# Performance work log

Measured on AMD Instinct MI355X. Metric: run time of the kernel, lower is better.

## Reference

```python
import jax, jax.numpy as jnp
import numpy as np

B, T, E, D = 32, 8192, 256, 32  # batch, seq, embed_dim, output_dim
H, M = D, 2 * D                 # SSM hidden_dim, mlp_dim


def _ssm_block(x, Win, bin_, log_a, Wout, bout, W1, b1, W2, b2):
    """Diagonal linear SSM scan + residual MLP. x: (B,T,D) -> (B,T,D)."""
    u = x @ Win + bin_                      # (B,T,H)
    a = jax.nn.sigmoid(log_a)               # (H,) per-channel decay in (0,1)
    aa = jnp.broadcast_to(a, u.shape)

    def comb(c1, c2):
        a1, h1 = c1
        a2, h2 = c2
        return a1 * a2, a2 * h1 + h2

    _, h = jax.lax.associative_scan(comb, (aa, u), axis=1)  # h_t = a*h_{t-1} + u_t
    y = h @ Wout + bout                      # (B,T,D)
    return y + jax.nn.gelu(y @ W1 + b1) @ W2 + b2


def setup_inputs() -> dict:
    key = jax.random.key(0)
    ks = jax.random.split(key, 20)
    s_in, s_d, s_m = 1.0 / np.sqrt(E), 1.0 / np.sqrt(D), 1.0 / np.sqrt(M)
    inp = {
        "e_seq": jax.random.normal(ks[0], (B, T, E), dtype=jnp.float32),
        "Wpi": jax.random.normal(ks[1], (E, D), dtype=jnp.float32) * s_in,
        "bpi": jnp.zeros((D,), jnp.float32),
        "Wpo": jax.random.normal(ks[2], (2 * D, D), dtype=jnp.float32) * s_d,
        "bpo": jnp.zeros((D,), jnp.float32),
    }
    for i, pfx in enumerate(["f", "b"]):
        o = 3 + 8 * i
        inp[pfx + "_Win"] = jax.random.normal(ks[o], (D, H), dtype=jnp.float32) * s_d
        inp[pfx + "_bin"] = jnp.zeros((H,), jnp.float32)
        inp[pfx + "_loga"] = jax.random.normal(ks[o + 1], (H,), dtype=jnp.float32)
        inp[pfx + "_Wout"] = jax.random.normal(ks[o + 2], (H, D), dtype=jnp.float32) * s_d
        inp[pfx + "_bout"] = jnp.zeros((D,), jnp.float32)
        inp[pfx + "_W1"] = jax.random.normal(ks[o + 3], (D, M), dtype=jnp.float32) * s_d
        inp[pfx + "_b1"] = jnp.zeros((M,), jnp.float32)
        inp[pfx + "_W2"] = jax.random.normal(ks[o + 4], (M, D), dtype=jnp.float32) * s_m
        inp[pfx + "_b2"] = jnp.zeros((D,), jnp.float32)
    return inp


def reference(e_seq, Wpi, bpi, Wpo, bpo,
              f_Win, f_bin, f_loga, f_Wout, f_bout, f_W1, f_b1, f_W2, f_b2,
              b_Win, b_bin, b_loga, b_Wout, b_bout, b_W1, b_b1, b_W2, b_b2):
    x = e_seq @ Wpi + bpi                                    # (B,T,D)
    fwd = _ssm_block(x, f_Win, f_bin, f_loga, f_Wout, f_bout, f_W1, f_b1, f_W2, f_b2)
    bwd = _ssm_block(x[:, ::-1], b_Win, b_bin, b_loga, b_Wout, b_bout,
                     b_W1, b_b1, b_W2, b_b2)[:, ::-1]
    combined = jnp.concatenate([fwd, bwd], axis=-1)           # (B,T,2D)
    return combined @ Wpo + bpo                               # (B,T,D)
```

## Files before the change

kernel.cpp:

```cpp
#include <hip/hip_runtime.h>


typedef unsigned short u16;
typedef unsigned int   u32;
typedef __bf16 bf16x8 __attribute__((ext_vector_type(8)));
typedef float  f32x4  __attribute__((ext_vector_type(4)));

constexpr int BB = 32, TT = 8192, EE = 256, DD = 32, NCH = 64;
constexpr int BT = BB * TT;
constexpr int LCH = 256;
constexpr int NCHUNK = TT / LCH;
constexpr int SUBLEN = 64;

__device__ __forceinline__ u16 f2bf(float x) {
    union { float f; u32 u; } v; v.f = x;
    u32 r = (v.u + 0x7FFFu + ((v.u >> 16) & 1u)) >> 16;
    return (u16)r;
}
__device__ __forceinline__ float bf2f(u16 x) {
    union { u32 u; float f; } v; v.u = ((u32)x) << 16;
    return v.f;
}
__device__ __forceinline__ float gelu_tanh(float x) {
    float inner = 0.7978845608028654f * fmaf(0.044715f * x, x * x, x);
    float ez = __expf(2.f * inner);
    float t = 1.f - 2.f / (ez + 1.f);
    return 0.5f * x * (1.f + t);
}

__global__ void k0_prep(const float* __restrict__ Wpi, const float* __restrict__ bpi,
                        const float* __restrict__ fWin, const float* __restrict__ fbin,
                        const float* __restrict__ floga,
                        const float* __restrict__ bWin, const float* __restrict__ bbin,
                        const float* __restrict__ bloga,
                        const float* __restrict__ fW1, const float* __restrict__ bW1,
                        const float* __restrict__ fW2, const float* __restrict__ bW2,
                        const float* __restrict__ fb2, const float* __restrict__ bb2,
                        const float* __restrict__ Wpo, const float* __restrict__ bpo,
                        u16* __restrict__ WuT, float* __restrict__ bu,
                        float* __restrict__ a_arr, float* __restrict__ l2a,
                        float* __restrict__ fW1T, float* __restrict__ bW1T,
                        float* __restrict__ W2poF, float* __restrict__ W2poB,
                        float* __restrict__ bc)
{
    const int blk = blockIdx.x, tid = threadIdx.x;
    if (blk < 64) {
        const float* Win = (blk < 32) ? fWin : bWin;
        const int nn = blk & 31;
        float s = 0.f;
        #pragma unroll
        for (int d = 0; d < 32; ++d) s = fmaf(Wpi[tid * 32 + d], Win[d * 32 + nn], s);
        WuT[blk * 256 + tid] = f2bf(s);
        if (tid == 0) {
            const float* bin = (blk < 32) ? fbin : bbin;
            float sb = bin[nn];
            for (int d = 0; d < 32; ++d) sb = fmaf(bpi[d], Win[d * 32 + nn], sb);
            bu[blk] = sb;
        }
    } else if (blk == 64) {
        if (tid < 64) {
            const float* lg = (tid < 32) ? floga : bloga;
            float a = 1.f / (1.f + __expf(-lg[tid & 31]));
            a_arr[tid] = a;
            l2a[tid] = log2f(a);
        } else if (tid < 96) {
            int i = tid - 64;
            float s = bpo[i];
            for (int d = 0; d < 32; ++d) s = fmaf(fb2[d], Wpo[d * 32 + i], s);
            for (int d = 0; d < 32; ++d) s = fmaf(bb2[d], Wpo[(32 + d) * 32 + i], s);
            bc[i] = s;
        }
    } else if (blk == 65 || blk == 66) {
        const float* W1 = (blk == 65) ? fW1 : bW1;
        float* W1T = (blk == 65) ? fW1T : bW1T;
        for (int x = tid; x < 2048; x += 256) {
            int j = x >> 5, i = x & 31;
            W1T[j * 32 + i] = W1[i * 64 + j];
        }
    } else {
        const float* W2 = (blk == 67) ? fW2 : bW2;
        const float* Wp = (blk == 67) ? Wpo : (Wpo + 32 * 32);
        float* Dst = (blk == 67) ? W2poF : W2poB;
        for (int x = tid; x < 2048; x += 256) {
            int j = x >> 5, i = x & 31;
            float s = 0.f;
            for (int d = 0; d < 32; ++d) s = fmaf(W2[j * 32 + d], Wp[d * 32 + i], s);
            Dst[j * 32 + i] = s;
        }
    }
}

__global__ __launch_bounds__(256) void k1_proj(const float* __restrict__ e,
                                               const u16* __restrict__ WuT,
                                               const float* __restrict__ bu,
                                               u16* __restrict__ u)
{
    __shared__ __align__(16) u16 As[64][264];
    const int tid = threadIdx.x;
    const size_t m0 = (size_t)blockIdx.x * 64;

    const float4* eg = reinterpret_cast<const float4*>(e + m0 * 256);
    #pragma unroll
    for (int it = 0; it < 16; ++it) {
        int i = tid + it * 256;
        int r = i >> 6, kk = (i & 63) << 2;
        float4 v = eg[i];
        uint2 pk;
        pk.x = (u32)f2bf(v.x) | ((u32)f2bf(v.y) << 16);
        pk.y = (u32)f2bf(v.z) | ((u32)f2bf(v.w) << 16);
        *reinterpret_cast<uint2*>(&As[r][kk]) = pk;
    }
    __syncthreads();

    const int lane = tid & 63, wave = tid >> 6;
    const int row16 = lane & 15, quad = lane >> 4;
    f32x4 acc[4] = {{0.f,0.f,0.f,0.f},{0.f,0.f,0.f,0.f},{0.f,0.f,0.f,0.f},{0.f,0.f,0.f,0.f}};

    #pragma unroll 2
    for (int ks = 0; ks < 8; ++ks) {
        bf16x8 av = *reinterpret_cast<const bf16x8*>(&As[wave * 16 + row16][ks * 32 + quad * 8]);
        #pragma unroll
        for (int ct = 0; ct < 4; ++ct) {
            bf16x8 bv = *reinterpret_cast<const bf16x8*>(WuT + (ct * 16 + row16) * 256 + ks * 32 + quad * 8);
            acc[ct] = __builtin_amdgcn_mfma_f32_16x16x32_bf16(av, bv, acc[ct], 0, 0, 0);
        }
    }
    #pragma unroll
    for (int ct = 0; ct < 4; ++ct) {
        int col = ct * 16 + row16;
        float bias = bu[col];
        #pragma unroll
        for (int r = 0; r < 4; ++r) {
            int row = wave * 16 + quad * 4 + r;
            u[(m0 + row) * 64 + col] = f2bf(acc[ct][r] + bias);
        }
    }
}

__global__ __launch_bounds__(256) void k2_scan(u16* __restrict__ u,
                                               const float* __restrict__ a_arr,
                                               const float* __restrict__ l2a,
                                               float* __restrict__ Ebuf)
{
    __shared__ __align__(16) u16 tile[LCH * 64];
    __shared__ float eSub[64][4];
    const int tid = threadIdx.x;
    const int b = blockIdx.x >> 5, c = blockIdx.x & 31;
    const size_t base = (((size_t)b << 13) + ((size_t)c << 8)) * 64;

    const uint4* g = reinterpret_cast<const uint4*>(u + base);
    uint4* s4 = reinterpret_cast<uint4*>(tile);
    #pragma unroll
    for (int i = 0; i < 8; ++i) s4[tid + 256 * i] = g[tid + 256 * i];
    __syncthreads();

    const int ch = tid & 63, s = tid >> 6;
    const float a = a_arr[ch];
    const bool fwd = (ch < 32);

    float h = 0.f;
    if (fwd) {
        for (int i = 0; i < SUBLEN; ++i) {
            int t = s * SUBLEN + i;
            h = fmaf(a, h, bf2f(tile[t * 64 + ch]));
            tile[t * 64 + ch] = f2bf(h);
        }
    } else {
        for (int i = SUBLEN - 1; i >= 0; --i) {
            int t = s * SUBLEN + i;
            h = fmaf(a, h, bf2f(tile[t * 64 + ch]));
            tile[t * 64 + ch] = f2bf(h);
        }
    }
    eSub[ch][s] = h;
    __syncthreads();

    const float A = exp2f(64.f * l2a[ch]);
    float cin = 0.f;
    if (fwd) { for (int j = 0; j < s; ++j)      cin = fmaf(A, cin, eSub[ch][j]); }
    else     { for (int j = 3; j > s; --j)      cin = fmaf(A, cin, eSub[ch][j]); }

    if (fwd && s == 3)  Ebuf[(size_t)blockIdx.x * 64 + ch] = fmaf(A, cin, eSub[ch][3]);
    if (!fwd && s == 0) Ebuf[(size_t)blockIdx.x * 64 + ch] = fmaf(A, cin, eSub[ch][0]);

    float p = cin;
    if (fwd) {
        for (int i = 0; i < SUBLEN; ++i) {
            int t = s * SUBLEN + i; p *= a;
            tile[t * 64 + ch] = f2bf(bf2f(tile[t * 64 + ch]) + p);
        }
    } else {
        for (int i = SUBLEN - 1; i >= 0; --i) {
            int t = s * SUBLEN + i; p *= a;
            tile[t * 64 + ch] = f2bf(bf2f(tile[t * 64 + ch]) + p);
        }
    }
    __syncthreads();
    uint4* gw = reinterpret_cast<uint4*>(u + base);
    #pragma unroll
    for (int i = 0; i < 8; ++i) gw[tid + 256 * i] = s4[tid + 256 * i];
}

__global__ void k3_carry(const float* __restrict__ Ebuf, float* __restrict__ Cin,
                         const float* __restrict__ l2a)
{
    int tid = blockIdx.x * 256 + threadIdx.x;
    if (tid >= BB * NCH) return;
    int b = tid >> 6, ch = tid & 63;
    float aL = exp2f((float)LCH * l2a[ch]);
    float S = 0.f;
    if (ch < 32) {
        for (int c = 0; c < NCHUNK; ++c) {
            size_t idx = ((size_t)(b * NCHUNK + c)) * 64 + ch;
            Cin[idx] = S; S = fmaf(aL, S, Ebuf[idx]);
        }
    } else {
        for (int c = NCHUNK - 1; c >= 0; --c) {
            size_t idx = ((size_t)(b * NCHUNK + c)) * 64 + ch;
            Cin[idx] = S; S = fmaf(aL, S, Ebuf[idx]);
        }
    }
}

__global__ __launch_bounds__(256) void k4_out(const u16* __restrict__ h,
    const float* __restrict__ Cin, const float* __restrict__ l2a,
    const float* __restrict__ fWout, const float* __restrict__ fbout,
    const float* __restrict__ fW1T, const float* __restrict__ fb1,
    const float* __restrict__ bWout, const float* __restrict__ bbout,
    const float* __restrict__ bW1T, const float* __restrict__ bb1,
    const float* __restrict__ W2poF, const float* __restrict__ W2poB,
    const float* __restrict__ bc, const float* __restrict__ Wpo,
    float* __restrict__ out)
{
    const int tid = threadIdx.x;
    const int k = tid;
    const size_t gt = (size_t)blockIdx.x * 256 + tid;
    const u16* hp = h + gt * 64;
    const float* cinp = Cin + (size_t)blockIdx.x * 64;

    float outacc[32];
    #pragma unroll
    for (int i = 0; i < 32; ++i) outacc[i] = bc[i];

    for (int dir = 0; dir < 2; ++dir) {
        const float* Wout = dir ? bWout : fWout;
        const float* bout = dir ? bbout : fbout;
        const float* W1T  = dir ? bW1T  : fW1T;
        const float* b1   = dir ? bb1   : fb1;
        const float* W2po = dir ? W2poB : W2poF;
        const int cb = dir ? 32 : 0;
        const float off = dir ? (float)(LCH - k) : (float)(k + 1);

        float yv[32];
        #pragma unroll
        for (int i = 0; i < 32; ++i) yv[i] = bout[i];
        for (int j0 = 0; j0 < 32; j0 += 8) {
            uint4 hv = *reinterpret_cast<const uint4*>(hp + cb + j0);
            u32 hw[4] = {hv.x, hv.y, hv.z, hv.w};
            #pragma unroll
            for (int jj = 0; jj < 8; ++jj) {
                const int j = j0 + jj;
                float hl = bf2f((u16)((hw[jj >> 1] >> ((jj & 1) * 16)) & 0xFFFFu));
                float hj = fmaf(cinp[cb + j], exp2f(off * l2a[cb + j]), hl);
                #pragma unroll
                for (int i = 0; i < 32; ++i) yv[i] = fmaf(hj, Wout[j * 32 + i], yv[i]);
            }
        }
        #pragma unroll
        for (int j = 0; j < 32; ++j) {
            #pragma unroll
            for (int i = 0; i < 32; ++i)
                outacc[i] = fmaf(yv[j], Wpo[(cb + j) * 32 + i], outacc[i]);
        }
        for (int j = 0; j < 64; ++j) {
            float z0 = b1[j], z1 = 0.f;
            #pragma unroll
            for (int i = 0; i < 16; ++i) z0 = fmaf(yv[i], W1T[j * 32 + i], z0);
            #pragma unroll
            for (int i = 16; i < 32; ++i) z1 = fmaf(yv[i], W1T[j * 32 + i], z1);
            float z = gelu_tanh(z0 + z1);
            #pragma unroll
            for (int i = 0; i < 32; ++i)
                outacc[i] = fmaf(z, W2po[j * 32 + i], outacc[i]);
        }
    }
    float4* op = reinterpret_cast<float4*>(out + gt * 32);
    #pragma unroll
    for (int q = 0; q < 8; ++q)
        op[q] = make_float4(outacc[4*q], outacc[4*q+1], outacc[4*q+2], outacc[4*q+3]);
}

extern "C" void kernel_launch(void* const* d_in, const int* in_sizes, int n_in,
                              void* d_out, int out_size, void* d_ws, size_t ws_size,
                              hipStream_t stream)
{
    (void)in_sizes; (void)n_in; (void)out_size; (void)ws_size;
    const float* e     = (const float*)d_in[0];
    const float* Wpi   = (const float*)d_in[1];
    const float* bpi   = (const float*)d_in[2];
    const float* Wpo   = (const float*)d_in[3];
    const float* bpo   = (const float*)d_in[4];
    const float* fWin  = (const float*)d_in[5];
    const float* fbin  = (const float*)d_in[6];
    const float* floga = (const float*)d_in[7];
    const float* fWout = (const float*)d_in[8];
    const float* fbout = (const float*)d_in[9];
    const float* fW1   = (const float*)d_in[10];
    const float* fb1   = (const float*)d_in[11];
    const float* fW2   = (const float*)d_in[12];
    const float* fb2   = (const float*)d_in[13];
    const float* bWin  = (const float*)d_in[14];
    const float* bbin  = (const float*)d_in[15];
    const float* bloga = (const float*)d_in[16];
    const float* bWout = (const float*)d_in[17];
    const float* bbout = (const float*)d_in[18];
    const float* bW1   = (const float*)d_in[19];
    const float* bb1   = (const float*)d_in[20];
    const float* bW2   = (const float*)d_in[21];
    const float* bb2   = (const float*)d_in[22];
    float* outp = (float*)d_out;

    char* ws = (char*)d_ws;
    size_t off = 0;
    auto walloc = [&](size_t bytes) { void* p = ws + off; off += (bytes + 255) & ~(size_t)255; return p; };
    u16*   u     = (u16*)  walloc((size_t)BT * 64 * 2);
    u16*   WuT   = (u16*)  walloc(64 * 256 * 2);
    float* bu    = (float*)walloc(64 * 4);
    float* a_arr = (float*)walloc(64 * 4);
    float* l2a   = (float*)walloc(64 * 4);
    float* Ebuf  = (float*)walloc((size_t)BB * NCHUNK * 64 * 4);
    float* Cin   = (float*)walloc((size_t)BB * NCHUNK * 64 * 4);
    float* fW1T  = (float*)walloc(64 * 32 * 4);
    float* bW1T  = (float*)walloc(64 * 32 * 4);
    float* W2poF = (float*)walloc(64 * 32 * 4);
    float* W2poB = (float*)walloc(64 * 32 * 4);
    float* bc    = (float*)walloc(32 * 4);

    k0_prep<<<69, 256, 0, stream>>>(Wpi, bpi, fWin, fbin, floga, bWin, bbin, bloga,
                                    fW1, bW1, fW2, bW2, fb2, bb2, Wpo, bpo,
                                    WuT, bu, a_arr, l2a, fW1T, bW1T, W2poF, W2poB, bc);
    k1_proj<<<BT / 64, 256, 0, stream>>>(e, WuT, bu, u);
    k2_scan<<<BB * NCHUNK, 256, 0, stream>>>(u, a_arr, l2a, Ebuf);
    k3_carry<<<8, 256, 0, stream>>>(Ebuf, Cin, l2a);
    k4_out<<<BB * NCHUNK, 256, 0, stream>>>(u, Cin, l2a,
                                            fWout, fbout, fW1T, fb1,
                                            bWout, bbout, bW1T, bb1,
                                            W2poF, W2poB, bc, Wpo, outp);
}
```

Baseline: 564.4 us.

## Fuse projection with chunk scan and move output MLP to bf16 MFMA

The input projection GEMM and the per-chunk scan now run in one kernel, so the u tensor stays in shared memory instead of taking a global write and re-read. The output kernel replaces per-thread scalar FP32 matmuls (Wout, W1, W2·Wpo, Wpo) with bf16 MFMA tiles. It stages y and the gelu activations in swizzled shared memory, and the prep kernel now builds transposed bf16 weight layouts for these products. Rounding y and z to bf16 adds some precision loss.

After: 463.4 us. 1.22x faster.

```diff
diff --git a/kernel.cpp b/kernel.cpp
--- a/kernel.cpp
+++ b/kernel.cpp
@@ -6,11 +6,12 @@
 typedef __bf16 bf16x8 __attribute__((ext_vector_type(8)));
 typedef float  f32x4  __attribute__((ext_vector_type(4)));
 
-constexpr int BB = 32, TT = 8192, EE = 256, DD = 32, NCH = 64;
+constexpr int BB = 32, TT = 8192, NCH = 64;
 constexpr int BT = BB * TT;
 constexpr int LCH = 256;
 constexpr int NCHUNK = TT / LCH;
-constexpr int SUBLEN = 64;
+
+#define MFMA16(av, bv, cc) __builtin_amdgcn_mfma_f32_16x16x32_bf16((av), (bv), (cc), 0, 0, 0)
 
 __device__ __forceinline__ u16 f2bf(float x) {
     union { float f; u32 u; } v; v.f = x;
@@ -36,11 +37,12 @@
                         const float* __restrict__ fW1, const float* __restrict__ bW1,
                         const float* __restrict__ fW2, const float* __restrict__ bW2,
                         const float* __restrict__ fb2, const float* __restrict__ bb2,
+                        const float* __restrict__ fWout, const float* __restrict__ bWout,
                         const float* __restrict__ Wpo, const float* __restrict__ bpo,
                         u16* __restrict__ WuT, float* __restrict__ bu,
                         float* __restrict__ a_arr, float* __restrict__ l2a,
-                        float* __restrict__ fW1T, float* __restrict__ bW1T,
-                        float* __restrict__ W2poF, float* __restrict__ W2poB,
+                        u16* __restrict__ W1Tbf, u16* __restrict__ W2poCatT,
+                        u16* __restrict__ WoutTbf, u16* __restrict__ WpoCatT,
                         float* __restrict__ bc)
 {
     const int blk = blockIdx.x, tid = threadIdx.x;
@@ -71,132 +73,120 @@
             bc[i] = s;
         }
     } else if (blk == 65 || blk == 66) {
-        const float* W1 = (blk == 65) ? fW1 : bW1;
-        float* W1T = (blk == 65) ? fW1T : bW1T;
+        int dir = blk - 65;
+        const float* W1 = dir ? bW1 : fW1;
         for (int x = tid; x < 2048; x += 256) {
-            int j = x >> 5, i = x & 31;
-            W1T[j * 32 + i] = W1[i * 64 + j];
-        }
-    } else {
-        const float* W2 = (blk == 67) ? fW2 : bW2;
-        const float* Wp = (blk == 67) ? Wpo : (Wpo + 32 * 32);
-        float* Dst = (blk == 67) ? W2poF : W2poB;
+            int n = x >> 5, k = x & 31;
+            W1Tbf[dir * 2048 + n * 32 + k] = f2bf(W1[k * 64 + n]);
+        }
+    } else if (blk == 67 || blk == 68) {
+        int dir = blk - 67;
+        const float* W2 = dir ? bW2 : fW2;
+        const float* Wp = Wpo + dir * 32 * 32;
         for (int x = tid; x < 2048; x += 256) {
             int j = x >> 5, i = x & 31;
             float s = 0.f;
             for (int d = 0; d < 32; ++d) s = fmaf(W2[j * 32 + d], Wp[d * 32 + i], s);
-            Dst[j * 32 + i] = s;
-        }
-    }
-}
-
-__global__ __launch_bounds__(256) void k1_proj(const float* __restrict__ e,
-                                               const u16* __restrict__ WuT,
-                                               const float* __restrict__ bu,
-                                               u16* __restrict__ u)
-{
-    __shared__ __align__(16) u16 As[64][264];
+            W2poCatT[i * 128 + dir * 64 + j] = f2bf(s);
+        }
+    } else if (blk == 69 || blk == 70) {
+        int dir = blk - 69;
+        const float* Wout = dir ? bWout : fWout;
+        for (int x = tid; x < 1024; x += 256) {
+            int n = x >> 5, k = x & 31;
+            WoutTbf[dir * 1024 + n * 32 + k] = f2bf(Wout[k * 32 + n]);
+        }
+    } else {
+        for (int x = tid; x < 2048; x += 256) {
+            int n = x >> 6, k = x & 63;
+            WpoCatT[n * 64 + k] = f2bf(Wpo[k * 32 + n]);
+        }
+    }
+}
+
+__global__ __launch_bounds__(256) void kA_proj_scan(const float* __restrict__ e,
+    const u16* __restrict__ WuT, const float* __restrict__ bu,
+    const float* __restrict__ a_arr, const float* __restrict__ l2a,
+    u16* __restrict__ h, float* __restrict__ Ebuf)
+{
+    __shared__ __align__(16) u16 As[32][264];
+    __shared__ __align__(16) u16 utile[256 * 64];
+    __shared__ float eSub[64][4];
     const int tid = threadIdx.x;
-    const size_t m0 = (size_t)blockIdx.x * 64;
-
-    const float4* eg = reinterpret_cast<const float4*>(e + m0 * 256);
-    #pragma unroll
-    for (int it = 0; it < 16; ++it) {
-        int i = tid + it * 256;
-        int r = i >> 6, kk = (i & 63) << 2;
-        float4 v = eg[i];
-        uint2 pk;
-        pk.x = (u32)f2bf(v.x) | ((u32)f2bf(v.y) << 16);
-        pk.y = (u32)f2bf(v.z) | ((u32)f2bf(v.w) << 16);
-        *reinterpret_cast<uint2*>(&As[r][kk]) = pk;
-    }
-    __syncthreads();
-
+    const int blk = blockIdx.x;
+    const size_t t0 = (size_t)blk * 256;
     const int lane = tid & 63, wave = tid >> 6;
     const int row16 = lane & 15, quad = lane >> 4;
-    f32x4 acc[4] = {{0.f,0.f,0.f,0.f},{0.f,0.f,0.f,0.f},{0.f,0.f,0.f,0.f},{0.f,0.f,0.f,0.f}};
-
-    #pragma unroll 2
-    for (int ks = 0; ks < 8; ++ks) {
-        bf16x8 av = *reinterpret_cast<const bf16x8*>(&As[wave * 16 + row16][ks * 32 + quad * 8]);
-        #pragma unroll
-        for (int ct = 0; ct < 4; ++ct) {
-            bf16x8 bv = *reinterpret_cast<const bf16x8*>(WuT + (ct * 16 + row16) * 256 + ks * 32 + quad * 8);
-            acc[ct] = __builtin_amdgcn_mfma_f32_16x16x32_bf16(av, bv, acc[ct], 0, 0, 0);
-        }
-    }
-    #pragma unroll
-    for (int ct = 0; ct < 4; ++ct) {
-        int col = ct * 16 + row16;
-        float bias = bu[col];
-        #pragma unroll
-        for (int r = 0; r < 4; ++r) {
-            int row = wave * 16 + quad * 4 + r;
-            u[(m0 + row) * 64 + col] = f2bf(acc[ct][r] + bias);
-        }
-    }
-}
-
-__global__ __launch_bounds__(256) void k2_scan(u16* __restrict__ u,
-                                               const float* __restrict__ a_arr,
-                                               const float* __restrict__ l2a,
-                                               float* __restrict__ Ebuf)
-{
-    __shared__ __align__(16) u16 tile[LCH * 64];
-    __shared__ float eSub[64][4];
-    const int tid = threadIdx.x;
-    const int b = blockIdx.x >> 5, c = blockIdx.x & 31;
-    const size_t base = (((size_t)b << 13) + ((size_t)c << 8)) * 64;
-
-    const uint4* g = reinterpret_cast<const uint4*>(u + base);
-    uint4* s4 = reinterpret_cast<uint4*>(tile);
-    #pragma unroll
-    for (int i = 0; i < 8; ++i) s4[tid + 256 * i] = g[tid + 256 * i];
-    __syncthreads();
-
-    const int ch = tid & 63, s = tid >> 6;
+    const int wr = (wave & 1) * 16;
+    const int wc = (wave >> 1) * 32;
+
+    #pragma unroll 1
+    for (int s = 0; s < 8; ++s) {
+        const float4* eg = reinterpret_cast<const float4*>(e + (t0 + s * 32) * 256);
+        #pragma unroll
+        for (int it = 0; it < 8; ++it) {
+            int i = tid + it * 256;
+            int r = i >> 6, kk = (i & 63) << 2;
+            float4 v = eg[i];
+            uint2 pk;
+            pk.x = (u32)f2bf(v.x) | ((u32)f2bf(v.y) << 16);
+            pk.y = (u32)f2bf(v.z) | ((u32)f2bf(v.w) << 16);
+            *reinterpret_cast<uint2*>(&As[r][kk]) = pk;
+        }
+        __syncthreads();
+        f32x4 acc[2] = {{0.f,0.f,0.f,0.f},{0.f,0.f,0.f,0.f}};
+        #pragma unroll
+        for (int ks = 0; ks < 8; ++ks) {
+            bf16x8 av = *reinterpret_cast<const bf16x8*>(&As[wr + row16][ks * 32 + quad * 8]);
+            #pragma unroll
+            for (int c2 = 0; c2 < 2; ++c2) {
+                bf16x8 bv = *reinterpret_cast<const bf16x8*>(WuT + (wc + c2 * 16 + row16) * 256 + ks * 32 + quad * 8);
+                acc[c2] = MFMA16(av, bv, acc[c2]);
+            }
+        }
+        #pragma unroll
+        for (int c2 = 0; c2 < 2; ++c2) {
+            int col = wc + c2 * 16 + row16;
+            float bias = bu[col];
+            #pragma unroll
+            for (int r = 0; r < 4; ++r) {
+                int trow = s * 32 + wr + quad * 4 + r;
+                utile[trow * 64 + col] = f2bf(acc[c2][r] + bias);
+            }
+        }
+        __syncthreads();
+    }
+
+    const int ch = tid & 63, sid = tid >> 6;
     const float a = a_arr[ch];
     const bool fwd = (ch < 32);
-
-    float h = 0.f;
+    float hh = 0.f;
     if (fwd) {
-        for (int i = 0; i < SUBLEN; ++i) {
-            int t = s * SUBLEN + i;
-            h = fmaf(a, h, bf2f(tile[t * 64 + ch]));
-            tile[t * 64 + ch] = f2bf(h);
-        }
+        for (int i = 0; i < 64; ++i) { int t = sid * 64 + i;
+            hh = fmaf(a, hh, bf2f(utile[t * 64 + ch])); utile[t * 64 + ch] = f2bf(hh); }
     } else {
-        for (int i = SUBLEN - 1; i >= 0; --i) {
-            int t = s * SUBLEN + i;
-            h = fmaf(a, h, bf2f(tile[t * 64 + ch]));
-            tile[t * 64 + ch] = f2bf(h);
-        }
-    }
-    eSub[ch][s] = h;
+        for (int i = 63; i >= 0; --i) { int t = sid * 64 + i;
+            hh = fmaf(a, hh, bf2f(utile[t * 64 + ch])); utile[t * 64 + ch] = f2bf(hh); }
+    }
+    eSub[ch][sid] = hh;
     __syncthreads();
-
     const float A = exp2f(64.f * l2a[ch]);
     float cin = 0.f;
-    if (fwd) { for (int j = 0; j < s; ++j)      cin = fmaf(A, cin, eSub[ch][j]); }
-    else     { for (int j = 3; j > s; --j)      cin = fmaf(A, cin, eSub[ch][j]); }
-
-    if (fwd && s == 3)  Ebuf[(size_t)blockIdx.x * 64 + ch] = fmaf(A, cin, eSub[ch][3]);
-    if (!fwd && s == 0) Ebuf[(size_t)blockIdx.x * 64 + ch] = fmaf(A, cin, eSub[ch][0]);
-
+    if (fwd) { for (int j = 0; j < sid; ++j) cin = fmaf(A, cin, eSub[ch][j]); }
+    else     { for (int j = 3; j > sid; --j) cin = fmaf(A, cin, eSub[ch][j]); }
+    if (fwd && sid == 3)  Ebuf[(size_t)blk * 64 + ch] = fmaf(A, cin, eSub[ch][3]);
+    if (!fwd && sid == 0) Ebuf[(size_t)blk * 64 + ch] = fmaf(A, cin, eSub[ch][0]);
     float p = cin;
     if (fwd) {
-        for (int i = 0; i < SUBLEN; ++i) {
-            int t = s * SUBLEN + i; p *= a;
-            tile[t * 64 + ch] = f2bf(bf2f(tile[t * 64 + ch]) + p);
-        }
+        for (int i = 0; i < 64; ++i) { int t = sid * 64 + i; p *= a;
+            utile[t * 64 + ch] = f2bf(bf2f(utile[t * 64 + ch]) + p); }
     } else {
-        for (int i = SUBLEN - 1; i >= 0; --i) {
-            int t = s * SUBLEN + i; p *= a;
-            tile[t * 64 + ch] = f2bf(bf2f(tile[t * 64 + ch]) + p);
-        }
+        for (int i = 63; i >= 0; --i) { int t = sid * 64 + i; p *= a;
+            utile[t * 64 + ch] = f2bf(bf2f(utile[t * 64 + ch]) + p); }
     }
     __syncthreads();
-    uint4* gw = reinterpret_cast<uint4*>(u + base);
+    uint4* gw = reinterpret_cast<uint4*>(h + t0 * 64);
+    const uint4* s4 = reinterpret_cast<const uint4*>(utile);
     #pragma unroll
     for (int i = 0; i < 8; ++i) gw[tid + 256 * i] = s4[tid + 256 * i];
 }
@@ -222,72 +212,112 @@
     }
 }
 
-__global__ __launch_bounds__(256) void k4_out(const u16* __restrict__ h,
+__global__ __launch_bounds__(256) void kB_out(const u16* __restrict__ h,
     const float* __restrict__ Cin, const float* __restrict__ l2a,
-    const float* __restrict__ fWout, const float* __restrict__ fbout,
-    const float* __restrict__ fW1T, const float* __restrict__ fb1,
-    const float* __restrict__ bWout, const float* __restrict__ bbout,
-    const float* __restrict__ bW1T, const float* __restrict__ bb1,
-    const float* __restrict__ W2poF, const float* __restrict__ W2poB,
-    const float* __restrict__ bc, const float* __restrict__ Wpo,
-    float* __restrict__ out)
-{
+    const u16* __restrict__ WoutTbf, const float* __restrict__ fbout, const float* __restrict__ bbout,
+    const u16* __restrict__ W1Tbf, const float* __restrict__ fb1, const float* __restrict__ bb1,
+    const u16* __restrict__ WpoCatT, const u16* __restrict__ W2poCatT,
+    const float* __restrict__ bc, float* __restrict__ out)
+{
+    __shared__ __align__(16) u16 Yt[256 * 64];
+    __shared__ __align__(16) u16 Zw[4][16 * 128];
     const int tid = threadIdx.x;
-    const int k = tid;
-    const size_t gt = (size_t)blockIdx.x * 256 + tid;
-    const u16* hp = h + gt * 64;
-    const float* cinp = Cin + (size_t)blockIdx.x * 64;
-
-    float outacc[32];
-    #pragma unroll
-    for (int i = 0; i < 32; ++i) outacc[i] = bc[i];
-
-    for (int dir = 0; dir < 2; ++dir) {
-        const float* Wout = dir ? bWout : fWout;
-        const float* bout = dir ? bbout : fbout;
-        const float* W1T  = dir ? bW1T  : fW1T;
-        const float* b1   = dir ? bb1   : fb1;
-        const float* W2po = dir ? W2poB : W2poF;
-        const int cb = dir ? 32 : 0;
-        const float off = dir ? (float)(LCH - k) : (float)(k + 1);
-
-        float yv[32];
-        #pragma unroll
-        for (int i = 0; i < 32; ++i) yv[i] = bout[i];
-        for (int j0 = 0; j0 < 32; j0 += 8) {
-            uint4 hv = *reinterpret_cast<const uint4*>(hp + cb + j0);
+    const int blk = blockIdx.x;
+    const size_t t0 = (size_t)blk * 256;
+    const int lane = tid & 63, wave = tid >> 6;
+    const int row16 = lane & 15, quad = lane >> 4;
+    const float* cinp = Cin + (size_t)blk * 64;
+
+    #pragma unroll 1
+    for (int rr = 0; rr < 4; ++rr) {
+        const int rt = wave * 4 + rr;
+        const int kpos = rt * 16 + row16;
+        #pragma unroll
+        for (int dir = 0; dir < 2; ++dir) {
+            uint4 hv = *reinterpret_cast<const uint4*>(h + (t0 + kpos) * 64 + dir * 32 + quad * 8);
             u32 hw[4] = {hv.x, hv.y, hv.z, hv.w};
-            #pragma unroll
-            for (int jj = 0; jj < 8; ++jj) {
-                const int j = j0 + jj;
-                float hl = bf2f((u16)((hw[jj >> 1] >> ((jj & 1) * 16)) & 0xFFFFu));
-                float hj = fmaf(cinp[cb + j], exp2f(off * l2a[cb + j]), hl);
+            const float off = dir ? (float)(LCH - kpos) : (float)(kpos + 1);
+            union { bf16x8 v; u16 s[8]; } af;
+            #pragma unroll
+            for (int j = 0; j < 8; ++j) {
+                int chn = dir * 32 + quad * 8 + j;
+                float f = bf2f((u16)((hw[j >> 1] >> ((j & 1) * 16)) & 0xFFFFu));
+                f = fmaf(cinp[chn], exp2f(off * l2a[chn]), f);
+                af.s[j] = f2bf(f);
+            }
+            f32x4 yv[2] = {{0.f,0.f,0.f,0.f},{0.f,0.f,0.f,0.f}};
+            #pragma unroll
+            for (int nt = 0; nt < 2; ++nt) {
+                bf16x8 bv = *reinterpret_cast<const bf16x8*>(WoutTbf + dir * 1024 + (nt * 16 + row16) * 32 + quad * 8);
+                yv[nt] = MFMA16(af.v, bv, yv[nt]);
+            }
+            const float* boutp = dir ? bbout : fbout;
+            #pragma unroll
+            for (int nt = 0; nt < 2; ++nt) {
+                float bb = boutp[nt * 16 + row16];
                 #pragma unroll
-                for (int i = 0; i < 32; ++i) yv[i] = fmaf(hj, Wout[j * 32 + i], yv[i]);
-            }
-        }
-        #pragma unroll
-        for (int j = 0; j < 32; ++j) {
-            #pragma unroll
-            for (int i = 0; i < 32; ++i)
-                outacc[i] = fmaf(yv[j], Wpo[(cb + j) * 32 + i], outacc[i]);
-        }
-        for (int j = 0; j < 64; ++j) {
-            float z0 = b1[j], z1 = 0.f;
-            #pragma unroll
-            for (int i = 0; i < 16; ++i) z0 = fmaf(yv[i], W1T[j * 32 + i], z0);
-            #pragma unroll
-            for (int i = 16; i < 32; ++i) z1 = fmaf(yv[i], W1T[j * 32 + i], z1);
-            float z = gelu_tanh(z0 + z1);
-            #pragma unroll
-            for (int i = 0; i < 32; ++i)
-                outacc[i] = fmaf(z, W2po[j * 32 + i], outacc[i]);
-        }
-    }
-    float4* op = reinterpret_cast<float4*>(out + gt * 32);
-    #pragma unroll
-    for (int q = 0; q < 8; ++q)
-        op[q] = make_float4(outacc[4*q], outacc[4*q+1], outacc[4*q+2], outacc[4*q+3]);
+                for (int r = 0; r < 4; ++r) {
+                    int row = rt * 16 + quad * 4 + r;
+                    int col = dir * 32 + nt * 16 + row16;
+                    int cs = (col >> 3) ^ (row & 7);
+                    Yt[row * 64 + cs * 8 + (col & 7)] = f2bf(yv[nt][r] + bb);
+                }
+            }
+        }
+    }
+
+    #pragma unroll 1
+    for (int rr = 0; rr < 4; ++rr) {
+        const int rt = wave * 4 + rr;
+        const int arow = rt * 16 + row16;
+        f32x4 o0 = {0.f,0.f,0.f,0.f}, o1 = {0.f,0.f,0.f,0.f};
+
+        #pragma unroll
+        for (int kb = 0; kb < 2; ++kb) {
+            int cs = (kb * 4 + quad) ^ (arow & 7);
+            bf16x8 av = *reinterpret_cast<const bf16x8*>(&Yt[arow * 64 + cs * 8]);
+            bf16x8 bv0 = *reinterpret_cast<const bf16x8*>(WpoCatT + (row16) * 64 + kb * 32 + quad * 8);
+            bf16x8 bv1 = *reinterpret_cast<const bf16x8*>(WpoCatT + (16 + row16) * 64 + kb * 32 + quad * 8);
+            o0 = MFMA16(av, bv0, o0);
+            o1 = MFMA16(av, bv1, o1);
+        }
+        #pragma unroll
+        for (int dir = 0; dir < 2; ++dir) {
+            int cs = (dir * 4 + quad) ^ (arow & 7);
+            bf16x8 av = *reinterpret_cast<const bf16x8*>(&Yt[arow * 64 + cs * 8]);
+            const float* b1p = dir ? bb1 : fb1;
+            #pragma unroll
+            for (int nt2 = 0; nt2 < 4; ++nt2) {
+                f32x4 z = {0.f,0.f,0.f,0.f};
+                bf16x8 bv = *reinterpret_cast<const bf16x8*>(W1Tbf + dir * 2048 + (nt2 * 16 + row16) * 32 + quad * 8);
+                z = MFMA16(av, bv, z);
+                float bb = b1p[nt2 * 16 + row16];
+                #pragma unroll
+                for (int r = 0; r < 4; ++r) {
+                    float zz = gelu_tanh(z[r] + bb);
+                    int zrow = quad * 4 + r;
+                    int zcol = dir * 64 + nt2 * 16 + row16;
+                    int zcs = (zcol >> 3) ^ (zrow & 7);
+                    Zw[wave][zrow * 128 + zcs * 8 + (zcol & 7)] = f2bf(zz);
+                }
+            }
+        }
+        #pragma unroll
+        for (int kb = 0; kb < 4; ++kb) {
+            int zcs = (kb * 4 + quad) ^ (row16 & 7);
+            bf16x8 av = *reinterpret_cast<const bf16x8*>(&Zw[wave][row16 * 128 + zcs * 8]);
+            bf16x8 bv0 = *reinterpret_cast<const bf16x8*>(W2poCatT + (row16) * 128 + kb * 32 + quad * 8);
+            bf16x8 bv1 = *reinterpret_cast<const bf16x8*>(W2poCatT + (16 + row16) * 128 + kb * 32 + quad * 8);
+            o0 = MFMA16(av, bv0, o0);
+            o1 = MFMA16(av, bv1, o1);
+        }
+        #pragma unroll
+        for (int r = 0; r < 4; ++r) {
+            size_t row = t0 + rt * 16 + quad * 4 + r;
+            out[row * 32 + row16]      = o0[r] + bc[row16];
+            out[row * 32 + 16 + row16] = o1[r] + bc[16 + row16];
+        }
+    }
 }
 
 extern "C" void kernel_launch(void* const* d_in, const int* in_sizes, int n_in,
@@ -323,27 +353,26 @@
     char* ws = (char*)d_ws;
     size_t off = 0;
     auto walloc = [&](size_t bytes) { void* p = ws + off; off += (bytes + 255) & ~(size_t)255; return p; };
-    u16*   u     = (u16*)  walloc((size_t)BT * 64 * 2);
+    u16*   hbuf  = (u16*)  walloc((size_t)BT * 64 * 2);
     u16*   WuT   = (u16*)  walloc(64 * 256 * 2);
     float* bu    = (float*)walloc(64 * 4);
     float* a_arr = (float*)walloc(64 * 4);
     float* l2a   = (float*)walloc(64 * 4);
     float* Ebuf  = (float*)walloc((size_t)BB * NCHUNK * 64 * 4);
     float* Cin   = (float*)walloc((size_t)BB * NCHUNK * 64 * 4);
-    float* fW1T  = (float*)walloc(64 * 32 * 4);
-    float* bW1T  = (float*)walloc(64 * 32 * 4);
-    float* W2poF = (float*)walloc(64 * 32 * 4);
-    float* W2poB = (float*)walloc(64 * 32 * 4);
+    u16*   W1Tbf    = (u16*)walloc(2 * 64 * 32 * 2);
+    u16*   W2poCatT = (u16*)walloc(32 * 128 * 2);
+    u16*   WoutTbf  = (u16*)walloc(2 * 32 * 32 * 2);
+    u16*   WpoCatT  = (u16*)walloc(32 * 64 * 2);
     float* bc    = (float*)walloc(32 * 4);
 
-    k0_prep<<<69, 256, 0, stream>>>(Wpi, bpi, fWin, fbin, floga, bWin, bbin, bloga,
-                                    fW1, bW1, fW2, bW2, fb2, bb2, Wpo, bpo,
-                                    WuT, bu, a_arr, l2a, fW1T, bW1T, W2poF, W2poB, bc);
-    k1_proj<<<BT / 64, 256, 0, stream>>>(e, WuT, bu, u);
-    k2_scan<<<BB * NCHUNK, 256, 0, stream>>>(u, a_arr, l2a, Ebuf);
+    k0_prep<<<72, 256, 0, stream>>>(Wpi, bpi, fWin, fbin, floga, bWin, bbin, bloga,
+                                    fW1, bW1, fW2, bW2, fb2, bb2, fWout, bWout, Wpo, bpo,
+                                    WuT, bu, a_arr, l2a, W1Tbf, W2poCatT, WoutTbf, WpoCatT, bc);
+    kA_proj_scan<<<BB * NCHUNK, 256, 0, stream>>>(e, WuT, bu, a_arr, l2a, hbuf, Ebuf);
     k3_carry<<<8, 256, 0, stream>>>(Ebuf, Cin, l2a);
-    k4_out<<<BB * NCHUNK, 256, 0, stream>>>(u, Cin, l2a,
-                                            fWout, fbout, fW1T, fb1,
-                                            bWout, bbout, bW1T, bb1,
-                                            W2poF, W2poB, bc, Wpo, outp);
-}
+    kB_out<<<BB * NCHUNK, 256, 0, stream>>>(hbuf, Cin, l2a,
+                                            WoutTbf, fbout, bbout,
+                                            W1Tbf, fb1, bb1,
+                                            WpoCatT, W2poCatT, bc, outp);
+}
```
